# Kernel tuning notes

Hardware: AMD Instinct MI355X
Metric: run time of the kernel (lower is better)

The kernel has to match this reference:

```python
import jax, jax.numpy as jnp
import numpy as np

NUM_BUCKETS = 32
MAX_DISTANCE = 128


def _relative_position_bucket(relative_position):
    # bidirectional=True variant of T5's bucketing
    n = -relative_position
    num_buckets = NUM_BUCKETS // 2
    ret = (n < 0).astype(jnp.int32) * num_buckets
    n = jnp.abs(n)
    max_exact = num_buckets // 2
    is_small = n < max_exact
    # log-spaced buckets for large distances
    val_if_large = max_exact + (
        jnp.log(jnp.maximum(n, 1).astype(jnp.float32) / max_exact)
        / np.log(MAX_DISTANCE / max_exact)
        * (num_buckets - max_exact)
    ).astype(jnp.int32)
    val_if_large = jnp.minimum(val_if_large, num_buckets - 1)
    return ret + jnp.where(is_small, n, val_if_large)


def setup_inputs() -> dict:
    key = jax.random.key(0)
    ks = jax.random.split(key, 6)
    B, S, D, H, DK = 4, 1024, 1024, 16, 64
    inner = H * DK
    s = 1.0 / np.sqrt(D).astype(np.float32)
    x = jax.random.normal(ks[0], (B, S, D), jnp.float32)
    Wq = jax.random.normal(ks[1], (D, inner), jnp.float32) * s
    Wk = jax.random.normal(ks[2], (D, inner), jnp.float32) * s
    Wv = jax.random.normal(ks[3], (D, inner), jnp.float32) * s
    Wo = jax.random.normal(ks[4], (inner, D), jnp.float32) * s
    rel_emb = jax.random.normal(ks[5], (NUM_BUCKETS, H), jnp.float32) * 0.02
    return {"x": x, "Wq": Wq, "Wk": Wk, "Wv": Wv, "Wo": Wo, "rel_emb": rel_emb}


def reference(x, Wq, Wk, Wv, Wo, rel_emb):
    B, S, D = x.shape
    H = rel_emb.shape[1]
    DK = Wq.shape[1] // H

    def shape_heads(t):  # [B,S,H*DK] -> [B,H,S,DK]
        return t.reshape(B, S, H, DK).transpose(0, 2, 1, 3)

    q = shape_heads(x @ Wq)
    k = shape_heads(x @ Wk)
    v = shape_heads(x @ Wv)

    # note: T5 does NOT scale by 1/sqrt(d_kv)
    scores = jnp.einsum("bhqd,bhkd->bhqk", q, k)

    pos = jnp.arange(S)
    rel = pos[None, :] - pos[:, None]            # memory - query
    bucket = _relative_position_bucket(rel)      # [S,S] int32
    bias = rel_emb[bucket].transpose(2, 0, 1)[None]  # [1,H,S,S]

    weights = jax.nn.softmax(scores + bias, axis=-1)
    ctx = jnp.einsum("bhqk,bhkd->bhqd", weights, v)
    ctx = ctx.transpose(0, 2, 1, 3).reshape(B, S, H * DK)
    return ctx @ Wo
```

## Files before the change

### kernel.cpp

```cpp
#include <hip/hip_runtime.h>
#include <math.h>

#define B_ 4
#define S_ 1024
#define D_ 1024
#define H_ 16
#define DK_ 64

typedef short bf16x8 __attribute__((ext_vector_type(8)));
typedef float f32x4 __attribute__((ext_vector_type(4)));

__device__ __forceinline__ unsigned short f2bf(float f) {
    unsigned int u = __float_as_uint(f);
    u = (u + 0x7FFFu + ((u >> 16) & 1u)) >> 16;
    return (unsigned short)u;
}

__device__ __forceinline__ float exp2_fast(float x) {
#if __has_builtin(__builtin_amdgcn_exp2f)
    return __builtin_amdgcn_exp2f(x);
#else
    return exp2f(x);
#endif
}

__device__ __forceinline__ int cvt_pk_bf16(float lo, float hi) {
    int r;
    asm("v_cvt_pk_bf16_f32 %0, %1, %2" : "=v"(r) : "v"(lo), "v"(hi));
    return r;
}

__device__ __forceinline__ void gl2lds16(const void* g, void* l) {
    typedef unsigned int u32;
    auto gp = (const __attribute__((address_space(1))) u32*)(unsigned long long)g;
    auto lp = (__attribute__((address_space(3))) u32*)(unsigned int)(unsigned long long)l;
    __builtin_amdgcn_global_load_lds(gp, lp, 16, 0, 0);
}

#define LOG2E 1.44269504f
#define BIAS_OFF 20.0f

__global__ __launch_bounds__(256) void conv_all(
    const float* __restrict__ x,
    const float* __restrict__ W0, const float* __restrict__ W1,
    const float* __restrict__ W2, const float* __restrict__ W3,
    unsigned short* __restrict__ xb, unsigned short* __restrict__ Wts)
{
    __shared__ float T[32][33];
    const int t = threadIdx.x;
    const int bid = blockIdx.x;

    if (bid < 4096) {
        int i = (bid * 256 + t) * 4;
        float4 v = *(const float4*)&x[i];
        ushort4 o;
        o.x = f2bf(v.x); o.y = f2bf(v.y); o.z = f2bf(v.z); o.w = f2bf(v.w);
        *(ushort4*)&xb[i] = o;
        return;
    }
    int tile = bid - 4096;
    const int mat = tile >> 10;
    tile &= 1023;
    const float* W = (mat == 0) ? W0 : (mat == 1) ? W1 : (mat == 2) ? W2 : W3;
    unsigned short* Wt = Wts + (size_t)mat * 1048576;
    const int k0 = (tile >> 5) * 32, n0 = (tile & 31) * 32;
    {
        int r = t >> 3, c4 = (t & 7) * 4;
        float4 v = *(const float4*)&W[(size_t)(k0 + r) * D_ + n0 + c4];
        T[r][c4 + 0] = v.x; T[r][c4 + 1] = v.y; T[r][c4 + 2] = v.z; T[r][c4 + 3] = v.w;
    }
    __syncthreads();
    {
        int rn = t >> 3, c4 = (t & 7) * 4;
        ushort4 o;
        o.x = f2bf(T[c4 + 0][rn]); o.y = f2bf(T[c4 + 1][rn]);
        o.z = f2bf(T[c4 + 2][rn]); o.w = f2bf(T[c4 + 3][rn]);
        *(ushort4*)&Wt[(size_t)(n0 + rn) * D_ + k0 + c4] = o;
    }
}

__global__ __launch_bounds__(256) void gemm_qkv(
    const unsigned short* __restrict__ xb,
    const unsigned short* __restrict__ Wts,
    unsigned short* __restrict__ Qb, unsigned short* __restrict__ Kb,
    unsigned short* __restrict__ Vtb)
{
    const int bid = blockIdx.x;
    const int by = bid & 31;
    const int t_ = bid >> 5;
    const int z = t_ >> 3;
    const int bx = t_ & 7;
    const unsigned short* Bt = Wts + (size_t)z * 1048576;

    __shared__ __align__(16) unsigned short Ast[2][128][32];
    __shared__ __align__(16) unsigned short Bst[2][128][32];

    const int tid = threadIdx.x;
    const int wave = tid >> 6, lane = tid & 63;
    const int quad = lane >> 4, l16 = lane & 15;
    const int wm = (wave & 1) * 64, wn = (wave >> 1) * 64;
    const int row0 = by * 128, col0 = bx * 128;
    const int lr = lane >> 2, lc = (lane & 3) * 8;

    f32x4 acc[4][4];
#pragma unroll
    for (int i = 0; i < 4; i++)
#pragma unroll
        for (int j = 0; j < 4; j++) acc[i][j] = 0;

    auto stage = [&](int sb, int k0) {
#pragma unroll
        for (int c = 0; c < 2; c++) {
            int m = wave * 32 + c * 16;
            gl2lds16(&xb[(size_t)(row0 + m + lr) * D_ + k0 + lc], &Ast[sb][m][0]);
            gl2lds16(&Bt[(size_t)(col0 + m + lr) * D_ + k0 + lc], &Bst[sb][m][0]);
        }
    };

    stage(0, 0);
    int db = 0;
    for (int k0 = 0; k0 < D_; k0 += 32) {
        __syncthreads();
        if (k0 + 32 < D_) stage(db ^ 1, k0 + 32);

        bf16x8 af[4], bfr[4];
#pragma unroll
        for (int mt = 0; mt < 4; mt++)
            af[mt] = *(const bf16x8*)&Ast[db][wm + mt * 16 + l16][quad * 8];
#pragma unroll
        for (int nt = 0; nt < 4; nt++)
            bfr[nt] = *(const bf16x8*)&Bst[db][wn + nt * 16 + l16][quad * 8];
#pragma unroll
        for (int mt = 0; mt < 4; mt++)
#pragma unroll
            for (int nt = 0; nt < 4; nt++)
                acc[mt][nt] = __builtin_amdgcn_mfma_f32_16x16x32_bf16(
                    af[mt], bfr[nt], acc[mt][nt], 0, 0, 0);
        db ^= 1;
    }

    const float scale = (z == 0) ? LOG2E : 1.0f;
#pragma unroll
    for (int mt = 0; mt < 4; mt++)
#pragma unroll
        for (int nt = 0; nt < 4; nt++)
#pragma unroll
            for (int reg = 0; reg < 4; reg++) {
                int row = row0 + wm + mt * 16 + quad * 4 + reg;
                int col = col0 + wn + nt * 16 + l16;
                int b = row >> 10, s = row & 1023;
                int h = col >> 6, dk = col & 63;
                unsigned short v = f2bf(acc[mt][nt][reg] * scale);
                if (z == 0)      Qb[(((size_t)(b * H_ + h)) * S_ + s) * DK_ + dk] = v;
                else if (z == 1) Kb[(((size_t)(b * H_ + h)) * S_ + s) * DK_ + dk] = v;
                else             Vtb[(((size_t)(b * H_ + h)) * DK_ + dk) * S_ + s] = v;
            }
}

__global__ __launch_bounds__(256) void gemm_out(
    const unsigned short* __restrict__ Ab,
    const unsigned short* __restrict__ Bt,
    float* __restrict__ out)
{
    const int bid = blockIdx.x;
    const int by = bid & 63;
    const int bx = bid >> 6;

    __shared__ __align__(16) unsigned short Ast[2][64][32];
    __shared__ __align__(16) unsigned short Bst[2][128][32];

    const int tid = threadIdx.x;
    const int wave = tid >> 6, lane = tid & 63;
    const int quad = lane >> 4, l16 = lane & 15;
    const int wm = (wave & 1) * 32, wn = (wave >> 1) * 64;
    const int row0 = by * 64, col0 = bx * 128;
    const int lr = lane >> 2, lc = (lane & 3) * 8;

    f32x4 acc[2][4];
#pragma unroll
    for (int i = 0; i < 2; i++)
#pragma unroll
        for (int j = 0; j < 4; j++) acc[i][j] = 0;

    auto stage = [&](int sb, int k0) {
        gl2lds16(&Ab[(size_t)(row0 + wave * 16 + lr) * D_ + k0 + lc],
                 &Ast[sb][wave * 16][0]);
#pragma unroll
        for (int c = 0; c < 2; c++) {
            int m = (wave * 2 + c) * 16;
            gl2lds16(&Bt[(size_t)(col0 + m + lr) * D_ + k0 + lc], &Bst[sb][m][0]);
        }
    };

    stage(0, 0);
    int db = 0;
    for (int k0 = 0; k0 < D_; k0 += 32) {
        __syncthreads();
        if (k0 + 32 < D_) stage(db ^ 1, k0 + 32);

        bf16x8 af[2], bfr[4];
#pragma unroll
        for (int mt = 0; mt < 2; mt++)
            af[mt] = *(const bf16x8*)&Ast[db][wm + mt * 16 + l16][quad * 8];
#pragma unroll
        for (int nt = 0; nt < 4; nt++)
            bfr[nt] = *(const bf16x8*)&Bst[db][wn + nt * 16 + l16][quad * 8];
#pragma unroll
        for (int mt = 0; mt < 2; mt++)
#pragma unroll
            for (int nt = 0; nt < 4; nt++)
                acc[mt][nt] = __builtin_amdgcn_mfma_f32_16x16x32_bf16(
                    af[mt], bfr[nt], acc[mt][nt], 0, 0, 0);
        db ^= 1;
    }

#pragma unroll
    for (int mt = 0; mt < 2; mt++)
#pragma unroll
        for (int nt = 0; nt < 4; nt++)
#pragma unroll
            for (int reg = 0; reg < 4; reg++) {
                int row = row0 + wm + mt * 16 + quad * 4 + reg;
                int col = col0 + wn + nt * 16 + l16;
                out[(size_t)row * D_ + col] = acc[mt][nt][reg];
            }
}

__global__ __launch_bounds__(256) void attn_mfma(
    const unsigned short* __restrict__ Qb, const unsigned short* __restrict__ Kb,
    const unsigned short* __restrict__ Vtb, const float* __restrict__ rel_emb,
    unsigned short* __restrict__ CTXb)
{
    __shared__ __align__(16) unsigned short Ks[3][64][64];
    __shared__ __align__(16) unsigned short Vts[3][64][64];
    __shared__ float bias_tab[2047];

    const int bid = blockIdx.x;
    const int bh = bid & 63;
    const int b = bh >> 4, h = bh & 15;
    const int q0 = (bid >> 6) * 128;
    const int tid = threadIdx.x;
    const int wave = tid >> 6, lane = tid & 63;
    const int quad = lane >> 4, l16 = lane & 15;
    const int qw = q0 + wave * 32;

    for (int idx = tid; idx < 2047; idx += 256) {
        int rel = idx - 1023;
        int n = -rel, ret = 0;
        if (n < 0) { ret = 16; n = -n; }
        int bkt;
        if (n < 8) bkt = ret + n;
        else {
            float t = logf((float)n / 8.0f) / logf(16.0f) * 8.0f;
            int v = 8 + (int)t;
            if (v > 15) v = 15;
            bkt = ret + v;
        }
        bias_tab[idx] = rel_emb[bkt * H_ + h] * LOG2E - BIAS_OFF;
    }

    const size_t hb = (size_t)(b * H_ + h) * (S_ * DK_);
    const unsigned short* Qp = Qb + hb;
    const unsigned short* Kp = Kb + hb;
    const unsigned short* Vp = Vtb + hb;

    bf16x8 qf[2][2];
#pragma unroll
    for (int sub = 0; sub < 2; sub++)
#pragma unroll
        for (int ks = 0; ks < 2; ks++)
            qf[sub][ks] = *(const bf16x8*)
                &Qp[(size_t)(qw + sub * 16 + l16) * DK_ + ks * 32 + quad * 8];

    f32x4 O[2][4];
#pragma unroll
    for (int sub = 0; sub < 2; sub++)
#pragma unroll
        for (int dt = 0; dt < 4; dt++) O[sub][dt] = 0;
    float lsum[2] = {0.f, 0.f};

    const int swz = l16 & 7;
    const int kr8 = lane >> 3;
    const int kck = ((lane & 7) ^ kr8) * 8;

    auto stageKV = [&](int sb, int kg) {
#pragma unroll
        for (int i = 0; i < 2; i++) {
            int blk = wave * 2 + i;
            gl2lds16(&Kp[(size_t)(kg + blk * 8 + kr8) * DK_ + kck],
                     &Ks[sb][blk * 8][0]);
            gl2lds16(&Vp[(size_t)(blk * 8 + kr8) * S_ + kg + kck],
                     &Vts[sb][blk * 8][0]);
        }
    };

    stageKV(0, 0);
    stageKV(1, 64);

    for (int kt = 0; kt < 16; kt++) {
        const int k0 = kt * 64;
        const int db = kt % 3;
        if (kt < 15) asm volatile("s_waitcnt vmcnt(4) lgkmcnt(0)" ::: "memory");
        else         asm volatile("s_waitcnt vmcnt(0) lgkmcnt(0)" ::: "memory");
        __builtin_amdgcn_s_barrier();
        __builtin_amdgcn_sched_barrier(0);
        if (kt < 14) stageKV((kt + 2) % 3, k0 + 128);

#pragma unroll
        for (int nt2 = 0; nt2 < 2; nt2++) {
            bf16x8 kf[2][2], vf[4];
#pragma unroll
            for (int t = 0; t < 2; t++) {
                int row = (2 * nt2 + t) * 16 + l16;
#pragma unroll
                for (int ks = 0; ks < 2; ks++)
                    kf[t][ks] = *(const bf16x8*)
                        &Ks[db][row][((ks * 4 + quad) ^ swz) * 8];
            }
#pragma unroll
            for (int dt = 0; dt < 4; dt++)
                vf[dt] = *(const bf16x8*)
                    &Vts[db][dt * 16 + l16][((nt2 * 4 + quad) ^ swz) * 8];

#pragma unroll
            for (int sub = 0; sub < 2; sub++) {
                f32x4 sacc[2];
#pragma unroll
                for (int t = 0; t < 2; t++) {
                    int b0 = 1023 + k0 + (2 * nt2 + t) * 16 + quad * 4
                             - (qw + sub * 16 + l16);
#pragma unroll
                    for (int reg = 0; reg < 4; reg++)
                        sacc[t][reg] = bias_tab[b0 + reg];
                }
                __builtin_amdgcn_s_setprio(1);
#pragma unroll
                for (int ks = 0; ks < 2; ks++)
#pragma unroll
                    for (int t = 0; t < 2; t++)
                        sacc[t] = __builtin_amdgcn_mfma_f32_16x16x32_bf16(
                            kf[t][ks], qf[sub][ks], sacc[t], 0, 0, 0);
                __builtin_amdgcn_s_setprio(0);

                float e0[4], e1[4];
#pragma unroll
                for (int reg = 0; reg < 4; reg++) {
                    e0[reg] = exp2_fast(sacc[0][reg]);
                    e1[reg] = exp2_fast(sacc[1][reg]);
                }
                lsum[sub] += (e0[0] + e0[1]) + (e0[2] + e0[3])
                           + (e1[0] + e1[1]) + (e1[2] + e1[3]);

                int x0 = cvt_pk_bf16(e0[0], e0[1]);
                int x1 = cvt_pk_bf16(e0[2], e0[3]);
                int x2 = cvt_pk_bf16(e1[0], e1[1]);
                int x3 = cvt_pk_bf16(e1[2], e1[3]);
                asm("v_permlane32_swap_b32 %0, %1" : "+v"(x0), "+v"(x2));
                asm("v_permlane32_swap_b32 %0, %1" : "+v"(x1), "+v"(x3));
                asm("v_permlane16_swap_b32 %0, %1" : "+v"(x0), "+v"(x2));
                asm("v_permlane16_swap_b32 %0, %1" : "+v"(x1), "+v"(x3));
                int4 pi; pi.x = x0; pi.y = x1; pi.z = x2; pi.w = x3;
                bf16x8 pf = __builtin_bit_cast(bf16x8, pi);

                __builtin_amdgcn_s_setprio(1);
#pragma unroll
                for (int dt = 0; dt < 4; dt++)
                    O[sub][dt] = __builtin_amdgcn_mfma_f32_16x16x32_bf16(
                        pf, vf[dt], O[sub][dt], 0, 0, 0);
                __builtin_amdgcn_s_setprio(0);
            }
        }
    }

#pragma unroll
    for (int sub = 0; sub < 2; sub++) {
        float l = lsum[sub];
        l += __shfl_xor(l, 16);
        l += __shfl_xor(l, 32);
        float invl = 1.0f / l;
#pragma unroll
        for (int reg = 0; reg < 4; reg++) {
            float inv = __shfl(invl, quad * 4 + reg);
            int s = qw + sub * 16 + quad * 4 + reg;
#pragma unroll
            for (int dt = 0; dt < 4; dt++) {
                int col = h * DK_ + dt * 16 + l16;
                CTXb[((size_t)(b * S_ + s)) * D_ + col] = f2bf(O[sub][dt][reg] * inv);
            }
        }
    }
}

extern "C" void kernel_launch(void* const* d_in, const int* in_sizes, int n_in,
                              void* d_out, int out_size, void* d_ws, size_t ws_size,
                              hipStream_t stream) {
    const float* x   = (const float*)d_in[0];
    const float* Wq  = (const float*)d_in[1];
    const float* Wk  = (const float*)d_in[2];
    const float* Wv  = (const float*)d_in[3];
    const float* Wo  = (const float*)d_in[4];
    const float* rel = (const float*)d_in[5];
    float* out = (float*)d_out;

    unsigned short* ws = (unsigned short*)d_ws;
    unsigned short* xb   = ws;
    unsigned short* Wts  = ws + (size_t)4194304;
    unsigned short* Qb   = ws + (size_t)8388608;
    unsigned short* Kb   = ws + (size_t)12582912;
    unsigned short* Vtb  = ws + (size_t)16777216;
    unsigned short* CTXb = ws + (size_t)20971520;

    conv_all<<<8192, 256, 0, stream>>>(x, Wq, Wk, Wv, Wo, xb, Wts);
    gemm_qkv<<<768, 256, 0, stream>>>(xb, Wts, Qb, Kb, Vtb);
    attn_mfma<<<512, 256, 0, stream>>>(Qb, Kb, Vtb, rel, CTXb);
    gemm_out<<<512, 256, 0, stream>>>(CTXb, Wts + (size_t)3 * 1048576, out);
}
```

Measured before the change: 169.1 us.

## Use per-block float4 bias window and MFMA ones-vector row sums

Replaces the full 2047-entry scalar bias table with a per-block window of 1152 float4 entries, each holding four consecutive biases. Each score tile then fetches its bias with one vector LDS load instead of four scalar loads. The softmax denominator now comes from an extra MFMA against a vector of bf16 ones, replacing the VALU sums and cross-lane shuffles. In exchange, the window table stores four times as many floats and computes the log-bucket four times per entry. The extra MFMA also sums the bf16-rounded probabilities, so the denominator matches the values fed to the PV product.

Result: no change. 169.2 us (+0.0%).

```diff
diff --git a/kernel.cpp b/kernel.cpp
--- a/kernel.cpp
+++ b/kernel.cpp
@@ -233,7 +233,7 @@
 {
     __shared__ __align__(16) unsigned short Ks[3][64][64];
     __shared__ __align__(16) unsigned short Vts[3][64][64];
-    __shared__ float bias_tab[2047];
+    __shared__ __align__(16) float4 tabW[1152];
 
     const int bid = blockIdx.x;
     const int bh = bid & 63;
@@ -244,19 +244,24 @@
     const int quad = lane >> 4, l16 = lane & 15;
     const int qw = q0 + wave * 32;
 
-    for (int idx = tid; idx < 2047; idx += 256) {
-        int rel = idx - 1023;
-        int n = -rel, ret = 0;
-        if (n < 0) { ret = 16; n = -n; }
-        int bkt;
-        if (n < 8) bkt = ret + n;
-        else {
-            float t = logf((float)n / 8.0f) / logf(16.0f) * 8.0f;
-            int v = 8 + (int)t;
-            if (v > 15) v = 15;
-            bkt = ret + v;
-        }
-        bias_tab[idx] = rel_emb[bkt * H_ + h] * LOG2E - BIAS_OFF;
+    for (int i = tid; i < 1152; i += 256) {
+        float4 v;
+#pragma unroll
+        for (int j = 0; j < 4; j++) {
+            int rel = i - (q0 + 127) + j;
+            int n = -rel, ret = 0;
+            if (n < 0) { ret = 16; n = -n; }
+            int bkt;
+            if (n < 8) bkt = ret + n;
+            else {
+                float t = logf((float)n / 8.0f) / logf(16.0f) * 8.0f;
+                int vv = 8 + (int)t;
+                if (vv > 15) vv = 15;
+                bkt = ret + vv;
+            }
+            (&v.x)[j] = rel_emb[bkt * H_ + h] * LOG2E - BIAS_OFF;
+        }
+        tabW[i] = v;
     }
 
     const size_t hb = (size_t)(b * H_ + h) * (S_ * DK_);
@@ -272,12 +277,17 @@
             qf[sub][ks] = *(const bf16x8*)
                 &Qp[(size_t)(qw + sub * 16 + l16) * DK_ + ks * 32 + quad * 8];
 
+    bf16x8 onesf;
+#pragma unroll
+    for (int j = 0; j < 8; j++) onesf[j] = (short)0x3F80;
+
     f32x4 O[2][4];
 #pragma unroll
     for (int sub = 0; sub < 2; sub++)
 #pragma unroll
         for (int dt = 0; dt < 4; dt++) O[sub][dt] = 0;
-    float lsum[2] = {0.f, 0.f};
+    f32x4 lacc[2];
+    lacc[0] = 0; lacc[1] = 0;
 
     const int swz = l16 & 7;
     const int kr8 = lane >> 3;
@@ -296,6 +306,8 @@
 
     stageKV(0, 0);
     stageKV(1, 64);
+
+    const int qoff = 127 - (wave * 32 + l16);
 
     for (int kt = 0; kt < 16; kt++) {
         const int k0 = kt * 64;
@@ -327,11 +339,11 @@
                 f32x4 sacc[2];
 #pragma unroll
                 for (int t = 0; t < 2; t++) {
-                    int b0 = 1023 + k0 + (2 * nt2 + t) * 16 + quad * 4
-                             - (qw + sub * 16 + l16);
-#pragma unroll
-                    for (int reg = 0; reg < 4; reg++)
-                        sacc[t][reg] = bias_tab[b0 + reg];
+                    int iw = qoff + k0 + (2 * nt2 + t) * 16 + quad * 4
+                             - sub * 16;
+                    float4 bl = tabW[iw];
+                    sacc[t][0] = bl.x; sacc[t][1] = bl.y;
+                    sacc[t][2] = bl.z; sacc[t][3] = bl.w;
                 }
                 __builtin_amdgcn_s_setprio(1);
 #pragma unroll
@@ -348,8 +360,6 @@
                     e0[reg] = exp2_fast(sacc[0][reg]);
                     e1[reg] = exp2_fast(sacc[1][reg]);
                 }
-                lsum[sub] += (e0[0] + e0[1]) + (e0[2] + e0[3])
-                           + (e1[0] + e1[1]) + (e1[2] + e1[3]);
 
                 int x0 = cvt_pk_bf16(e0[0], e0[1]);
                 int x1 = cvt_pk_bf16(e0[2], e0[3]);
@@ -367,20 +377,18 @@
                 for (int dt = 0; dt < 4; dt++)
                     O[sub][dt] = __builtin_amdgcn_mfma_f32_16x16x32_bf16(
                         pf, vf[dt], O[sub][dt], 0, 0, 0);
+                lacc[sub] = __builtin_amdgcn_mfma_f32_16x16x32_bf16(
+                    pf, onesf, lacc[sub], 0, 0, 0);
                 __builtin_amdgcn_s_setprio(0);
             }
         }
     }
 
 #pragma unroll
-    for (int sub = 0; sub < 2; sub++) {
-        float l = lsum[sub];
-        l += __shfl_xor(l, 16);
-        l += __shfl_xor(l, 32);
-        float invl = 1.0f / l;
+    for (int sub = 0; sub < 2; sub++)
 #pragma unroll
         for (int reg = 0; reg < 4; reg++) {
-            float inv = __shfl(invl, quad * 4 + reg);
+            float inv = 1.0f / lacc[sub][reg];
             int s = qw + sub * 16 + quad * 4 + reg;
 #pragma unroll
             for (int dt = 0; dt < 4; dt++) {
@@ -388,7 +396,6 @@
                 CTXb[((size_t)(b * S_ + s)) * D_ + col] = f2bf(O[sub][dt][reg] * inv);
             }
         }
-    }
 }
 
 extern "C" void kernel_launch(void* const* d_in, const int* in_sizes, int n_in,
```
